# Performance work log

Measured on AMD Instinct MI355X. Metric: run time of the kernel, lower is better.

Reference implementation:

```python
import jax, jax.numpy as jnp
import numpy as np
import math

W = 64  # window_size == chunk_size == 64


def _windows(x, w):
    """x: [b, t, ...] -> [b, nb, 2w, ...]: for block j, concat(block j-1, block j).
    Block -1 is zero padding; its validity is handled by the attention mask."""
    b, t = x.shape[0], x.shape[1]
    nb = t // w
    pad = [(0, 0), (w, 0)] + [(0, 0)] * (x.ndim - 2)
    xp = jnp.pad(x, pad)                                   # [b, t+w, ...]
    xb = xp.reshape((b, nb + 1, w) + x.shape[2:])          # [b, nb+1, w, ...]
    return jnp.concatenate([xb[:, :-1], xb[:, 1:]], axis=2)  # [b, nb, 2w, ...]


def setup_inputs() -> dict:
    key = jax.random.key(0)
    k1, k2, k3 = jax.random.split(key, 3)
    b, t, h, d = 4, 4096, 16, 64
    return {
        "q": jax.random.normal(k1, (b, t, h, d), dtype=jnp.float32),
        "k": jax.random.normal(k2, (b, t, h, d), dtype=jnp.float32),
        "v": jax.random.normal(k3, (b, t, h, d), dtype=jnp.float32),
        "attn_mask": jnp.ones((b, t), dtype=jnp.int32),
    }


def reference(q, k, v, attn_mask):
    b, t, h, d = q.shape
    nb = t // W
    scale = 1.0 / math.sqrt(d)

    qb = q.reshape(b, nb, W, h, d)
    kw = _windows(k, W)                         # [b, nb, 2W, h, d]
    vw = _windows(v, W)                         # [b, nb, 2W, h, d]
    mw = _windows(attn_mask.astype(bool), W)    # [b, nb, 2W]

    # query local index i attends to key local index m iff 0 <= (i+W-m) < W
    i = jnp.arange(W)[:, None]
    m = jnp.arange(2 * W)[None, :]
    diff = i + W - m
    band = (diff >= 0) & (diff < W)             # [W, 2W]

    valid = band[None, None] & mw[:, :, None, :]          # [b, nb, W, 2W]

    scores = jnp.einsum('bnqhd,bnkhd->bnhqk', qb, kw) * scale  # [b,nb,h,W,2W]
    scores = jnp.where(valid[:, :, None], scores, jnp.float32(-1e9))
    attn = jax.nn.softmax(scores, axis=-1)
    attn = attn * valid[:, :, None].astype(attn.dtype)

    qm = attn_mask.astype(q.dtype).reshape(b, nb, W)      # query validity
    attn = attn * qm[:, :, None, :, None]

    out = jnp.einsum('bnhqk,bnkhd->bnqhd', attn, vw)      # [b,nb,W,h,d]
    out = out * qm[:, :, :, None, None]
    return out.reshape(b, t, h, d)
```

## Files before the change

kernel.cpp:

```cpp
#include <hip/hip_runtime.h>
#include <hip/hip_bf16.h>


#define TT 4096
#define HH 16
#define DD 64
#define WW 64
#define NBLK (TT / WW)

typedef __attribute__((ext_vector_type(8))) short bf16x8;
typedef __attribute__((ext_vector_type(4))) float f32x4;

static __device__ __forceinline__ ushort f2bf(float x) {
    return __builtin_bit_cast(unsigned short, __float2bfloat16(x));
}

__global__ __launch_bounds__(256, 2)
void lca_fwd(const float* __restrict__ q, const float* __restrict__ k,
             const float* __restrict__ v, const int* __restrict__ am,
             float* __restrict__ out)
{
    const int jb = blockIdx.x;
    const int hi = blockIdx.y;
    const int bi = blockIdx.z;

    __shared__ ushort sQ[64][72];
    __shared__ ushort sK[128][72];
    __shared__ ushort sVt[64][136];
    __shared__ ushort sP[64][136];
    __shared__ int    sKv[128];
    __shared__ int    sQv[64];

    const int tid = threadIdx.x;
    const size_t rowstride = (size_t)HH * DD;
    const size_t qbase = ((size_t)(bi * TT + jb * WW) * HH + hi) * DD;
    const long  kstart = (long)jb * WW - WW;

    #pragma unroll
    for (int p = 0; p < 4; ++p) {
        int idx = p * 256 + tid;
        int row = idx >> 4, c4 = (idx & 15) * 4;
        float4 f = *(const float4*)(q + qbase + (size_t)row * rowstride + c4);
        uint2 u;
        u.x = (uint)f2bf(f.x) | ((uint)f2bf(f.y) << 16);
        u.y = (uint)f2bf(f.z) | ((uint)f2bf(f.w) << 16);
        *(uint2*)(&sQ[row][c4]) = u;
    }
    #pragma unroll
    for (int p = 0; p < 8; ++p) {
        int idx = p * 256 + tid;
        int row = idx >> 4, c4 = (idx & 15) * 4;
        long tok = kstart + row;
        float4 f = make_float4(0.f, 0.f, 0.f, 0.f);
        if (tok >= 0)
            f = *(const float4*)(k + ((size_t)(bi * TT + tok) * HH + hi) * DD + c4);
        uint2 u;
        u.x = (uint)f2bf(f.x) | ((uint)f2bf(f.y) << 16);
        u.y = (uint)f2bf(f.z) | ((uint)f2bf(f.w) << 16);
        *(uint2*)(&sK[row][c4]) = u;
    }
    #pragma unroll
    for (int p = 0; p < 8; ++p) {
        int idx = p * 256 + tid;
        int row = idx >> 4, c4 = (idx & 15) * 4;
        long tok = kstart + row;
        float4 f = make_float4(0.f, 0.f, 0.f, 0.f);
        if (tok >= 0)
            f = *(const float4*)(v + ((size_t)(bi * TT + tok) * HH + hi) * DD + c4);
        sVt[c4 + 0][row] = f2bf(f.x);
        sVt[c4 + 1][row] = f2bf(f.y);
        sVt[c4 + 2][row] = f2bf(f.z);
        sVt[c4 + 3][row] = f2bf(f.w);
    }
    if (tid < 128) {
        long tok = kstart + tid;
        sKv[tid] = (tok >= 0) && (am[(size_t)bi * TT + tok] != 0);
    } else if (tid < 192) {
        int r = tid - 128;
        sQv[r] = (am[(size_t)bi * TT + jb * WW + r] != 0);
    }
    __syncthreads();

    const int wv = tid >> 6, lane = tid & 63;
    const int quad = lane >> 4, l15 = lane & 15;
    const int r0 = 16 * wv + quad * 4;

    bf16x8 aq0 = *(const bf16x8*)(&sQ[16 * wv + l15][quad * 8]);
    bf16x8 aq1 = *(const bf16x8*)(&sQ[16 * wv + l15][32 + quad * 8]);

    f32x4 acc[8];
    #pragma unroll
    for (int kt = 0; kt < 8; ++kt) {
        f32x4 a = {0.f, 0.f, 0.f, 0.f};
        bf16x8 b0 = *(const bf16x8*)(&sK[16 * kt + l15][quad * 8]);
        bf16x8 b1 = *(const bf16x8*)(&sK[16 * kt + l15][32 + quad * 8]);
        a = __builtin_amdgcn_mfma_f32_16x16x32_bf16(aq0, b0, a, 0, 0, 0);
        a = __builtin_amdgcn_mfma_f32_16x16x32_bf16(aq1, b1, a, 0, 0, 0);
        acc[kt] = a;
    }

    const float NEG = -1.0e9f;
    float rmax[4] = {NEG, NEG, NEG, NEG};
    #pragma unroll
    for (int kt = 0; kt < 8; ++kt) {
        int c = 16 * kt + l15;
        int kvc = sKv[c];
        #pragma unroll
        for (int reg = 0; reg < 4; ++reg) {
            int r = r0 + reg;
            bool valid = (c > r) && (c <= r + WW) && kvc;
            float s = valid ? acc[kt][reg] : NEG;
            acc[kt][reg] = s;
            rmax[reg] = fmaxf(rmax[reg], s);
        }
    }
    #pragma unroll
    for (int reg = 0; reg < 4; ++reg) {
        #pragma unroll
        for (int m = 1; m <= 8; m <<= 1)
            rmax[reg] = fmaxf(rmax[reg], __shfl_xor(rmax[reg], m, 64));
    }

    const float CEXP = 0.125f * 1.44269504088896f;
    float rsum[4] = {0.f, 0.f, 0.f, 0.f};
    #pragma unroll
    for (int kt = 0; kt < 8; ++kt) {
        int c = 16 * kt + l15;
        #pragma unroll
        for (int reg = 0; reg < 4; ++reg) {
            float s = acc[kt][reg];
            float pex = (s > -1.0e8f) ? exp2f((s - rmax[reg]) * CEXP) : 0.f;
            rsum[reg] += pex;
            sP[r0 + reg][c] = f2bf(pex);
        }
    }
    float rden[4];
    #pragma unroll
    for (int reg = 0; reg < 4; ++reg) {
        #pragma unroll
        for (int m = 1; m <= 8; m <<= 1)
            rsum[reg] += __shfl_xor(rsum[reg], m, 64);
        rden[reg] = (rsum[reg] > 0.f ? 1.f / rsum[reg] : 0.f)
                    * (float)sQv[r0 + reg];
    }

    __syncthreads();

    bf16x8 ap[4];
    #pragma unroll
    for (int kc = 0; kc < 4; ++kc)
        ap[kc] = *(const bf16x8*)(&sP[16 * wv + l15][kc * 32 + quad * 8]);

    #pragma unroll
    for (int nt = 0; nt < 4; ++nt) {
        f32x4 a = {0.f, 0.f, 0.f, 0.f};
        #pragma unroll
        for (int kc = 0; kc < 4; ++kc) {
            bf16x8 bv = *(const bf16x8*)(&sVt[16 * nt + l15][kc * 32 + quad * 8]);
            a = __builtin_amdgcn_mfma_f32_16x16x32_bf16(ap[kc], bv, a, 0, 0, 0);
        }
        #pragma unroll
        for (int reg = 0; reg < 4; ++reg)
            out[qbase + (size_t)(r0 + reg) * rowstride + 16 * nt + l15]
                = a[reg] * rden[reg];
    }
}

extern "C" void kernel_launch(void* const* d_in, const int* in_sizes, int n_in,
                              void* d_out, int out_size, void* d_ws, size_t ws_size,
                              hipStream_t stream) {
    const float* q  = (const float*)d_in[0];
    const float* k  = (const float*)d_in[1];
    const float* v  = (const float*)d_in[2];
    const int*   am = (const int*)d_in[3];
    float* out = (float*)d_out;

    const int b = in_sizes[3] / TT;
    dim3 grid(NBLK, HH, b);
    dim3 block(256);
    lca_fwd<<<grid, block, 0, stream>>>(q, k, v, am, out);
}
```

Measured before the change: 284.5 us.

## Alias Q/K and P shared buffers, batch global loads, raise occupancy to 3

Q/K staging and the probability matrix P now share one LDS region through a union, with a barrier after the QK MFMAs so P can overwrite them. This cuts per-block LDS and lets the launch bound ask for three resident blocks per CU instead of two. All Q/K/V global loads are issued into registers before any bf16 conversion, and the jb>0 path drops the per-row bounds check, so more memory requests are in flight at once. The barrier before reading P is removed because each wave reads only rows it wrote itself. The cost is more live registers under a tighter register budget, which risks spills.

```diff
diff --git a/kernel.cpp b/kernel.cpp
--- a/kernel.cpp
+++ b/kernel.cpp
@@ -14,8 +14,11 @@
 static __device__ __forceinline__ ushort f2bf(float x) {
     return __builtin_bit_cast(unsigned short, __float2bfloat16(x));
 }
-
-__global__ __launch_bounds__(256, 2)
+static __device__ __forceinline__ uint pack2(float a, float b) {
+    return (uint)f2bf(a) | ((uint)f2bf(b) << 16);
+}
+
+__global__ __launch_bounds__(256, 3)
 void lca_fwd(const float* __restrict__ q, const float* __restrict__ k,
              const float* __restrict__ v, const int* __restrict__ am,
              float* __restrict__ out)
@@ -24,10 +27,11 @@
     const int hi = blockIdx.y;
     const int bi = blockIdx.z;
 
-    __shared__ ushort sQ[64][72];
-    __shared__ ushort sK[128][72];
+    __shared__ union {
+        struct { ushort Q[64][72]; ushort K[128][72]; } qk;
+        ushort P[64][136];
+    } u;
     __shared__ ushort sVt[64][136];
-    __shared__ ushort sP[64][136];
     __shared__ int    sKv[128];
     __shared__ int    sQv[64];
 
@@ -36,42 +40,6 @@
     const size_t qbase = ((size_t)(bi * TT + jb * WW) * HH + hi) * DD;
     const long  kstart = (long)jb * WW - WW;
 
-    #pragma unroll
-    for (int p = 0; p < 4; ++p) {
-        int idx = p * 256 + tid;
-        int row = idx >> 4, c4 = (idx & 15) * 4;
-        float4 f = *(const float4*)(q + qbase + (size_t)row * rowstride + c4);
-        uint2 u;
-        u.x = (uint)f2bf(f.x) | ((uint)f2bf(f.y) << 16);
-        u.y = (uint)f2bf(f.z) | ((uint)f2bf(f.w) << 16);
-        *(uint2*)(&sQ[row][c4]) = u;
-    }
-    #pragma unroll
-    for (int p = 0; p < 8; ++p) {
-        int idx = p * 256 + tid;
-        int row = idx >> 4, c4 = (idx & 15) * 4;
-        long tok = kstart + row;
-        float4 f = make_float4(0.f, 0.f, 0.f, 0.f);
-        if (tok >= 0)
-            f = *(const float4*)(k + ((size_t)(bi * TT + tok) * HH + hi) * DD + c4);
-        uint2 u;
-        u.x = (uint)f2bf(f.x) | ((uint)f2bf(f.y) << 16);
-        u.y = (uint)f2bf(f.z) | ((uint)f2bf(f.w) << 16);
-        *(uint2*)(&sK[row][c4]) = u;
-    }
-    #pragma unroll
-    for (int p = 0; p < 8; ++p) {
-        int idx = p * 256 + tid;
-        int row = idx >> 4, c4 = (idx & 15) * 4;
-        long tok = kstart + row;
-        float4 f = make_float4(0.f, 0.f, 0.f, 0.f);
-        if (tok >= 0)
-            f = *(const float4*)(v + ((size_t)(bi * TT + tok) * HH + hi) * DD + c4);
-        sVt[c4 + 0][row] = f2bf(f.x);
-        sVt[c4 + 1][row] = f2bf(f.y);
-        sVt[c4 + 2][row] = f2bf(f.z);
-        sVt[c4 + 3][row] = f2bf(f.w);
-    }
     if (tid < 128) {
         long tok = kstart + tid;
         sKv[tid] = (tok >= 0) && (am[(size_t)bi * TT + tok] != 0);
@@ -79,25 +47,93 @@
         int r = tid - 128;
         sQv[r] = (am[(size_t)bi * TT + jb * WW + r] != 0);
     }
+
+    float4 fq[4], fk[8], fv[8];
+    #pragma unroll
+    for (int p = 0; p < 4; ++p) {
+        int idx = p * 256 + tid;
+        int row = idx >> 4, c4 = (idx & 15) * 4;
+        fq[p] = *(const float4*)(q + qbase + (size_t)row * rowstride + c4);
+    }
+    if (jb > 0) {
+        #pragma unroll
+        for (int p = 0; p < 8; ++p) {
+            int idx = p * 256 + tid;
+            int row = idx >> 4, c4 = (idx & 15) * 4;
+            fk[p] = *(const float4*)(k + ((size_t)(bi * TT + kstart + row) * HH + hi) * DD + c4);
+        }
+        #pragma unroll
+        for (int p = 0; p < 8; ++p) {
+            int idx = p * 256 + tid;
+            int row = idx >> 4, c4 = (idx & 15) * 4;
+            fv[p] = *(const float4*)(v + ((size_t)(bi * TT + kstart + row) * HH + hi) * DD + c4);
+        }
+    } else {
+        #pragma unroll
+        for (int p = 0; p < 8; ++p) {
+            float4 z = make_float4(0.f, 0.f, 0.f, 0.f);
+            if (p >= 4) {
+                int idx = p * 256 + tid;
+                int row = idx >> 4, c4 = (idx & 15) * 4;
+                z = *(const float4*)(k + ((size_t)(bi * TT + (row - 64)) * HH + hi) * DD + c4);
+            }
+            fk[p] = z;
+        }
+        #pragma unroll
+        for (int p = 0; p < 8; ++p) {
+            float4 z = make_float4(0.f, 0.f, 0.f, 0.f);
+            if (p >= 4) {
+                int idx = p * 256 + tid;
+                int row = idx >> 4, c4 = (idx & 15) * 4;
+                z = *(const float4*)(v + ((size_t)(bi * TT + (row - 64)) * HH + hi) * DD + c4);
+            }
+            fv[p] = z;
+        }
+    }
+
+    #pragma unroll
+    for (int p = 0; p < 4; ++p) {
+        int idx = p * 256 + tid;
+        int row = idx >> 4, c4 = (idx & 15) * 4;
+        uint2 w; w.x = pack2(fq[p].x, fq[p].y); w.y = pack2(fq[p].z, fq[p].w);
+        *(uint2*)(&u.qk.Q[row][c4]) = w;
+    }
+    #pragma unroll
+    for (int p = 0; p < 8; ++p) {
+        int idx = p * 256 + tid;
+        int row = idx >> 4, c4 = (idx & 15) * 4;
+        uint2 w; w.x = pack2(fk[p].x, fk[p].y); w.y = pack2(fk[p].z, fk[p].w);
+        *(uint2*)(&u.qk.K[row][c4]) = w;
+    }
+    #pragma unroll
+    for (int p = 0; p < 8; ++p) {
+        int idx = p * 256 + tid;
+        int row = idx >> 4, c4 = (idx & 15) * 4;
+        sVt[c4 + 0][row] = f2bf(fv[p].x);
+        sVt[c4 + 1][row] = f2bf(fv[p].y);
+        sVt[c4 + 2][row] = f2bf(fv[p].z);
+        sVt[c4 + 3][row] = f2bf(fv[p].w);
+    }
     __syncthreads();
 
     const int wv = tid >> 6, lane = tid & 63;
     const int quad = lane >> 4, l15 = lane & 15;
     const int r0 = 16 * wv + quad * 4;
 
-    bf16x8 aq0 = *(const bf16x8*)(&sQ[16 * wv + l15][quad * 8]);
-    bf16x8 aq1 = *(const bf16x8*)(&sQ[16 * wv + l15][32 + quad * 8]);
+    bf16x8 aq0 = *(const bf16x8*)(&u.qk.Q[16 * wv + l15][quad * 8]);
+    bf16x8 aq1 = *(const bf16x8*)(&u.qk.Q[16 * wv + l15][32 + quad * 8]);
 
     f32x4 acc[8];
     #pragma unroll
     for (int kt = 0; kt < 8; ++kt) {
         f32x4 a = {0.f, 0.f, 0.f, 0.f};
-        bf16x8 b0 = *(const bf16x8*)(&sK[16 * kt + l15][quad * 8]);
-        bf16x8 b1 = *(const bf16x8*)(&sK[16 * kt + l15][32 + quad * 8]);
+        bf16x8 b0 = *(const bf16x8*)(&u.qk.K[16 * kt + l15][quad * 8]);
+        bf16x8 b1 = *(const bf16x8*)(&u.qk.K[16 * kt + l15][32 + quad * 8]);
         a = __builtin_amdgcn_mfma_f32_16x16x32_bf16(aq0, b0, a, 0, 0, 0);
         a = __builtin_amdgcn_mfma_f32_16x16x32_bf16(aq1, b1, a, 0, 0, 0);
         acc[kt] = a;
     }
+    __syncthreads();
 
     const float NEG = -1.0e9f;
     float rmax[4] = {NEG, NEG, NEG, NEG};
@@ -131,7 +167,7 @@
             float s = acc[kt][reg];
             float pex = (s > -1.0e8f) ? exp2f((s - rmax[reg]) * CEXP) : 0.f;
             rsum[reg] += pex;
-            sP[r0 + reg][c] = f2bf(pex);
+            u.P[r0 + reg][c] = f2bf(pex);
         }
     }
     float rden[4];
@@ -144,12 +180,10 @@
                     * (float)sQv[r0 + reg];
     }
 
-    __syncthreads();
-
     bf16x8 ap[4];
     #pragma unroll
     for (int kc = 0; kc < 4; ++kc)
-        ap[kc] = *(const bf16x8*)(&sP[16 * wv + l15][kc * 32 + quad * 8]);
+        ap[kc] = *(const bf16x8*)(&u.P[16 * wv + l15][kc * 32 + quad * 8]);
 
     #pragma unroll
     for (int nt = 0; nt < 4; ++nt) {
```

Measured after the change: 228.5 us. -19.7%, faster.
